# Kernel optimization log

Measured on AMD Instinct MI355X. Metric: run time of the kernel, lower is better.

The kernel has to match this reference:

```python
import jax, jax.numpy as jnp
import numpy as np

TAU = 0.01
RHO = 1.99
SIGMA = 1.0 / TAU / 72.0  # 1/tau/72 as in __init__
N_IT = 10  # n_it_max


def nabla2(x):
    # forward finite differences: channel 0 along W (last axis), channel 1 along H
    u = jnp.zeros(x.shape + (2,), x.dtype)
    u = u.at[..., :, :-1, 0].add(x[..., :, 1:] - x[..., :, :-1])
    u = u.at[..., :-1, :, 1].add(x[..., 1:, :] - x[..., :-1, :])
    return u


def nabla2_adjoint(u):
    x = jnp.zeros(u.shape[:-1], u.dtype)
    x = x.at[..., :, :-1].add(-u[..., :, :-1, 0])
    x = x.at[..., :, 1:].add(u[..., :, :-1, 0])
    x = x.at[..., :-1, :].add(-u[..., :-1, :, 1])
    x = x.at[..., 1:, :].add(u[..., :-1, :, 1])
    return x


def epsilon2(I):
    # Jacobian of the vector field I [..., H, W, 2] -> G [..., H, W, 4]
    I0, I1 = I[..., 0], I[..., 1]
    G = jnp.zeros(I0.shape + (4,), I.dtype)
    G = G.at[..., 0].add(I0)                                  # G0 = I0 - shift_H(I0)
    G = G.at[..., 1:, :, 0].add(-I0[..., :-1, :])
    G = G.at[..., :, 1:, 1].add(I0[..., :, 1:] - I0[..., :, :-1])  # G1: W-diff of I0
    G = G.at[..., 2].add(I1)                                  # G2 = I1 - shift_W(I1)
    G = G.at[..., :, 1:, 2].add(-I1[..., :, :-1])
    G = G.at[..., :-1, :, 3].add(I1[..., 1:, :] - I1[..., :-1, :])  # G3: H-diff of I1
    return G


def epsilon2_adjoint(G):
    I = jnp.zeros(G.shape[:-1] + (2,), G.dtype)
    I = I.at[..., 0].add(G[..., 0])
    I = I.at[..., :-1, :, 0].add(-G[..., 1:, :, 0])
    I = I.at[..., :, :-1, 0].add(-G[..., :, 1:, 1])
    I = I.at[..., :, 1:, 0].add(G[..., :, 1:, 1])
    I = I.at[..., 1].add(G[..., 2])
    I = I.at[..., :, :-1, 1].add(-G[..., :, 1:, 2])
    I = I.at[..., :-1, :, 1].add(-G[..., :-1, :, 3])
    I = I.at[..., 1:, :, 1].add(G[..., :-1, :, 3])
    return I


def setup_inputs() -> dict:
    key = jax.random.key(0)
    y = jax.random.normal(key, (4, 512, 512), dtype=jnp.float32)
    return {"y": y, "ths": 1}


def reference(y, ths):
    lam1 = ths * 0.1
    lam2 = ths * 0.15

    def prox_tau_fr(r):
        left = jnp.sqrt(jnp.sum(r * r, axis=-1)) / (TAU * lam1)
        return r - r / jnp.maximum(left, 1.0)[..., None]

    def prox_sigma_g_conj(u):
        return u / jnp.maximum(jnp.sqrt(jnp.sum(u * u, axis=-1)) / lam2, 1.0)[..., None]

    x2 = y
    r2 = jnp.zeros(y.shape + (2,), y.dtype)
    u2 = jnp.zeros(y.shape + (4,), y.dtype)

    def step(carry, _):
        x2, r2, u2 = carry
        tmp = TAU * epsilon2_adjoint(u2)
        x = (x2 - nabla2_adjoint(tmp) + TAU * y) / (1.0 + TAU)  # prox_tau_fx
        r = prox_tau_fr(r2 + tmp)
        u = prox_sigma_g_conj(
            u2 + SIGMA * epsilon2(nabla2(2.0 * x - x2) - (2.0 * r - r2))
        )
        x2 = x2 + RHO * (x - x2)
        r2 = r2 + RHO * (r - r2)
        u2 = u2 + RHO * (u - u2)
        return (x2, r2, u2), None

    (x2, r2, u2), _ = jax.lax.scan(step, (x2, r2, u2), None, length=N_IT)
    return x2
```

## Files before the change

### kernel.cpp

```cpp
#include <hip/hip_runtime.h>
#include <hip/hip_fp16.h>
#include <math.h>

#define HH 512
#define WW 512
#define BB 4
#define NPIX (BB * HH * WW)

#define HS 4
#define NSX 9
#define NBAND (HH / HS)
#define NWAVES (NSX * NBAND * BB)
#define NBLK (NWAVES / 4)
#define BPR (NBLK / 8)

constexpr float TAUf   = 0.01f;
constexpr float RHOf   = 1.99f;
constexpr float SIGMAf = (float)(1.0 / 0.01 / 72.0);
constexpr float INV1PT = (float)(1.0 / 1.01);

__device__ __forceinline__ float SD(float v) { return __shfl_down(v, 1, 64); }
__device__ __forceinline__ unsigned SDu(unsigned v) { return __shfl_down(v, 1, 64); }
__device__ __forceinline__ float SUp(float v) { return __shfl_up(v, 1, 64); }

__device__ __forceinline__ int swiz_wid(int bid, int tid) {
    return (((bid & 7) * BPR) + (bid >> 3)) * 4 + (tid >> 6);
}


template <int MODE>
__global__ __launch_bounds__(256) void sweep(
    const float* __restrict__ y, const int* __restrict__ ths_p,
    const uint2* __restrict__ f_in, const uint2* __restrict__ u_in,
    uint2* __restrict__ f_out, uint2* __restrict__ u_out,
    float* __restrict__ xout)
{
    const int tid  = threadIdx.x;
    const int lane = tid & 63;
    const int wid  = swiz_wid(blockIdx.x, tid);
    const int sx   = wid % NSX;
    const int t2   = wid / NSX;
    const int band = t2 & (NBAND - 1);
    const int b    = t2 / NBAND;
    const int R0   = band * HS;
    const int w    = sx * 60 - 2 + lane;
    const int boff = b * (HH * WW);
    const bool wok = ((unsigned)w) < (unsigned)WW;
    const float mA = (w >= 1 && w < WW) ? 1.f : 0.f;
    const float mB = (w >= 0 && w < WW - 1) ? 1.f : 0.f;
    const bool cok = (lane >= 2) && (lane < 62) && (w < WW);

    const float ths  = (float)ths_p[0];
    const float tl1_ = TAUf * (ths * 0.1f);
    const float l2_  = ths * 0.15f;

    float uf0[4], uf1[4], uf2[4], uf3[4];
    unsigned u12r[4];
    float i0r[2], i1r[2];
    float sr[2], t1r[2];
    float v0r[4], v1r[2];
    #pragma unroll
    for (int q = 0; q < 4; ++q) { uf0[q]=uf1[q]=uf2[q]=uf3[q]=0.f; v0r[q]=0.f; u12r[q]=0u; }
    i0r[0]=i0r[1]=i1r[0]=i1r[1]=0.f;
    sr[0]=sr[1]=0.f; t1r[0]=t1r[1]=0.f; v1r[0]=v1r[1]=0.f;

    auto uload = [&](int row) -> uint2 {
        uint2 z; z.x = 0u; z.y = 0u;
        if (((unsigned)row) < (unsigned)HH && wok)
            z = u_in[(size_t)(boff + row * WW + w)];
        return z;
    };
    auto fload = [&](int row) -> uint2 {
        uint2 z; z.x = 0u; z.y = 0u;
        if (((unsigned)row) < (unsigned)HH && wok)
            z = f_in[(size_t)(boff + row * WW + w)];
        return z;
    };
    auto unpk = [&](int slot, uint2 raw) {
        __half2 lo = *(reinterpret_cast<__half2*>(&raw.x));
        __half2 hi = *(reinterpret_cast<__half2*>(&raw.y));
        uf0[slot] = __low2float(lo); uf1[slot] = __high2float(lo);
        uf2[slot] = __low2float(hi); uf3[slot] = __high2float(hi);
        u12r[slot] = (raw.x >> 16) | (raw.y << 16);
    };
    auto compI = [&](int rr, int islot, int c, int d, int uu_) {
        if (((unsigned)rr) < (unsigned)HH) {
            float hD  = (rr < HH - 1) ? 1.f : 0.f;
            unsigned pp = SDu(u12r[c]);
            __half2 ph = *(reinterpret_cast<__half2*>(&pp));
            float u1n = __low2float(ph);
            float u2n = __high2float(ph);
            i0r[islot] = uf0[c] - uf0[d] - u1n + mA * uf1[c];
            i1r[islot] = uf2[c] - u2n - hD * uf3[c] + uf3[uu_];
        } else { i0r[islot] = 0.f; i1r[islot] = 0.f; }
    };

    if (MODE == 2) {
        unpk(2, uload(R0 - 2));
        unpk(3, uload(R0 - 1));
        unpk(0, uload(R0));
        compI(R0 - 1, 1, 3, 0, 2);
        uint2 puA = uload(R0 + 1);
        uint2 puB = uload(R0 + 2);
        uint2 pfA = fload(R0);
        uint2 pfB = fload(R0 + 1);
        #pragma unroll
        for (int k = 0; k < HS; ++k) {
            const int rr = R0 + k;
            unpk((k + 1) & 3, puA);
            puA = puB;
            if (k < HS - 2) puB = uload(R0 + k + 3);
            __half2 lo = *(reinterpret_cast<__half2*>(&pfA.x));
            __half2 hi = *(reinterpret_cast<__half2*>(&pfA.y));
            float x2v = __low2float(lo);
            float yv  = __high2float(hi);
            pfA = pfB;
            if (k < HS - 2) pfB = fload(R0 + k + 2);
            compI(rr, k & 1, k & 3, (k + 1) & 3, (k + 3) & 3);
            float hD = (rr < HH - 1) ? 1.f : 0.f;
            float i0c = i0r[k & 1], i1c = i1r[k & 1], i1u = i1r[(k + 1) & 1];
            float i0l = SUp(i0c);
            float na = TAUf * (mA * i0l - mB * i0c + i1u - hD * i1c);
            float x = (x2v - na + TAUf * yv) * INV1PT;
            if (cok) xout[boff + rr * WW + w] = x2v + RHOf * (x - x2v);
        }
        return;
    }

    auto compS = [&](int rr, int isc, int isp,
                     float yv, float x2v, float r20v, float r21v, unsigned yraw,
                     bool coreRow, float &sOut, float &t0Out, float &t1Out) {
        if (((unsigned)rr) < (unsigned)HH) {
            float hD = (rr < HH - 1) ? 1.f : 0.f;
            float i0c = i0r[isc], i1c = i1r[isc], i1u = i1r[isp];
            float i0l = SUp(i0c);
            float na = TAUf * (mA * i0l - mB * i0c + i1u - hD * i1c);
            float x = (x2v - na + TAUf * yv) * INV1PT;
            float rr0 = r20v + TAUf * i0c;
            float rr1 = r21v + TAUf * i1c;
            float d = rr0 * rr0 + rr1 * rr1;
            float rinv = fminf(tl1_ * __builtin_amdgcn_rsqf(d), 1.0f);
            float r0 = rr0 - rr0 * rinv;
            float r1 = rr1 - rr1 * rinv;
            sOut  = 2.f * x  - x2v;
            t0Out = 2.f * r0 - r20v;
            t1Out = 2.f * r1 - r21v;
            if (coreRow && cok) {
                int idx = boff + rr * WW + w;
                __half2 lo2 = __floats2half2_rn(x2v + RHOf * (x - x2v),
                                                r20v + RHOf * (r0 - r20v));
                unsigned r1b = (unsigned)__half_as_ushort(
                    __float2half(r21v + RHOf * (r1 - r21v)));
                uint2 st; st.x = *(unsigned*)&lo2; st.y = r1b | (yraw << 16);
                f_out[(size_t)idx] = st;
            }
        } else { sOut = 0.f; t0Out = 0.f; t1Out = 0.f; }
    };

    auto compU = [&](int ro, int v0c_s, int v0u_s, int v1c_s, int v1d_s, int uslot) {
        float hD  = (ro < HH - 1) ? 1.f : 0.f;
        float v0c = v0r[v0c_s], v0u = v0r[v0u_s];
        float v1c = v1r[v1c_s], v1d = v1r[v1d_s];
        float v0l = SUp(v0c);
        float v1l = SUp(v1c);
        float G0 = v0c - v0u;
        float G1 = mA * (v0c - v0l);
        float G2 = v1c - mA * v1l;
        float G3 = hD * (v1d - v1c);
        float u0v = uf0[uslot], u1v = uf1[uslot], u2v = uf2[uslot], u3v = uf3[uslot];
        float uu0 = u0v + SIGMAf * G0;
        float uu1 = u1v + SIGMAf * G1;
        float uu2 = u2v + SIGMAf * G2;
        float uu3 = u3v + SIGMAf * G3;
        float d = uu0 * uu0 + uu1 * uu1 + uu2 * uu2 + uu3 * uu3;
        float ui = fminf(l2_ * __builtin_amdgcn_rsqf(d), 1.0f);
        if (cok) {
            int idx = boff + ro * WW + w;
            __half2 lo = __floats2half2_rn(u0v + RHOf * (uu0 * ui - u0v),
                                           u1v + RHOf * (uu1 * ui - u1v));
            __half2 hi = __floats2half2_rn(u2v + RHOf * (uu2 * ui - u2v),
                                           u3v + RHOf * (uu3 * ui - u3v));
            uint2 st; st.x = *(unsigned*)&lo; st.y = *(unsigned*)&hi;
            u_out[(size_t)idx] = st;
        }
    };

    uint2 puA, puB, pfA, pfB;
    puA.x = puA.y = puB.x = puB.y = 0u;
    pfA.x = pfA.y = pfB.x = pfB.y = 0u;
    unpk(1, uload(R0 - 3));
    unpk(2, uload(R0 - 2));
    unpk(3, uload(R0 - 1));
    compI(R0 - 2, 0, 2, 3, 1);
    puA = uload(R0);
    puB = uload(R0 + 1);
    pfA = fload(R0 - 1);
    pfB = fload(R0);

    #pragma unroll
    for (int k = 0; k < HS + 3; ++k) {
        const int rr = R0 - 1 + k;
        unpk(k & 3, puA);
        puA = puB;
        if (k <= HS) puB = uload(R0 + k + 2);
        __half2 lo = *(reinterpret_cast<__half2*>(&pfA.x));
        __half2 hi = *(reinterpret_cast<__half2*>(&pfA.y));
        float x2v  = __low2float(lo);
        float r20v = __high2float(lo);
        float r21v = __low2float(hi);
        float yv   = __high2float(hi);
        unsigned yraw = pfA.y >> 16;
        pfA = pfB;
        if (k <= HS) pfB = fload(R0 + k + 1);

        compI(rr, (k + 1) & 1, (k + 3) & 3, k & 3, (k + 2) & 3);

        float sN, t0N, t1N;
        compS(rr, (k + 1) & 1, k & 1, yv, x2v, r20v, r21v, yraw,
              (k >= 1 && k <= HS), sN, t0N, t1N);

        {
            float sPrev  = sr[k & 1];
            float t1Prev = t1r[k & 1];
            float hDm1   = (rr < HH) ? 1.f : 0.f;
            v0r[(k + 3) & 3] = mB * (SD(sN) - sN) - t0N;
            v1r[k & 1]       = hDm1 * (sN - sPrev) - t1Prev;
            sr[(k + 1) & 1]  = sN;
            t1r[(k + 1) & 1] = t1N;
        }

        if (k >= 3) compU(R0 - 3 + k, (k + 1) & 3, k & 3, (k + 1) & 1, k & 1,
                          (k + 1) & 3);
    }
}

__global__ __launch_bounds__(256) void fused01(
    const float* __restrict__ y, const int* __restrict__ ths_p,
    uint2* __restrict__ f_out, uint2* __restrict__ u_out)
{
    const int tid  = threadIdx.x;
    const int lane = tid & 63;
    const int wid  = swiz_wid(blockIdx.x, tid);
    const int sx   = wid % NSX;
    const int t2   = wid / NSX;
    const int band = t2 & (NBAND - 1);
    const int b    = t2 / NBAND;
    const int R0   = band * HS;
    const int w    = sx * 58 - 3 + lane;
    const int boff = b * (HH * WW);
    const bool wok = ((unsigned)w) < (unsigned)WW;
    const float mA = (w >= 1 && w < WW) ? 1.f : 0.f;
    const float mB = (w >= 0 && w < WW - 1) ? 1.f : 0.f;
    const bool cok = (lane >= 3) && (lane <= 60) && (w < WW);

    const float ths  = (float)ths_p[0];
    const float tl1_ = TAUf * (ths * 0.1f);
    const float l2_  = ths * 0.15f;

    float p0r[4];
    float p1r[2];
    float yD1 = 0.f, yD2 = 0.f, yD3 = 0.f;

    float uf0[4], uf1[4], uf2[4], uf3[4];
    unsigned u12r[4];
    float i0r[2], i1r[2];
    float sr[2], t1r[2];
    float v0r[4], v1r[2];
    #pragma unroll
    for (int q = 0; q < 4; ++q) {
        uf0[q]=uf1[q]=uf2[q]=uf3[q]=0.f; v0r[q]=0.f; u12r[q]=0u; p0r[q]=0.f;
    }
    i0r[0]=i0r[1]=i1r[0]=i1r[1]=0.f;
    sr[0]=sr[1]=0.f; t1r[0]=t1r[1]=0.f; v1r[0]=v1r[1]=0.f; p1r[0]=p1r[1]=0.f;

    auto yload = [&](int row) -> float {
        return (((unsigned)row) < (unsigned)HH && wok)
                   ? y[boff + row * WW + w] : 0.f;
    };
    auto unpk = [&](int slot, uint2 raw) {
        __half2 lo = *(reinterpret_cast<__half2*>(&raw.x));
        __half2 hi = *(reinterpret_cast<__half2*>(&raw.y));
        uf0[slot] = __low2float(lo); uf1[slot] = __high2float(lo);
        uf2[slot] = __low2float(hi); uf3[slot] = __high2float(hi);
        u12r[slot] = (raw.x >> 16) | (raw.y << 16);
    };
    auto compI = [&](int rr, int islot, int c, int d, int uu_) {
        if (((unsigned)rr) < (unsigned)HH) {
            float hD  = (rr < HH - 1) ? 1.f : 0.f;
            unsigned pp = SDu(u12r[c]);
            __half2 ph = *(reinterpret_cast<__half2*>(&pp));
            float u1n = __low2float(ph);
            float u2n = __high2float(ph);
            i0r[islot] = uf0[c] - uf0[d] - u1n + mA * uf1[c];
            i1r[islot] = uf2[c] - u2n - hD * uf3[c] + uf3[uu_];
        } else { i0r[islot] = 0.f; i1r[islot] = 0.f; }
    };

    float pyA = yload(R0 - 4);
    float pyB = yload(R0 - 3);

    #pragma unroll
    for (int j = 0; j < HS + 9; ++j) {
        const int p = R0 - 4 + j;
        float yp = pyA; pyA = pyB;
        if (j <= HS + 6) pyB = yload(R0 - 2 + j);

        p0r[j & 3]       = mB * (SD(yp) - yp);
        p1r[(j + 1) & 1] = ((p < HH) ? 1.f : 0.f) * (yp - yD1);

        if (j >= 3) {
            const int ro = R0 - 6 + j;
            float hD  = (ro < HH - 1) ? 1.f : 0.f;
            float v0c = p0r[(j + 2) & 3], v0u = p0r[(j + 1) & 3];
            float v1c = p1r[j & 1],       v1d = p1r[(j + 1) & 1];
            float G0 = v0c - v0u;
            float G1 = mA * (v0c - SUp(v0c));
            float G2 = v1c - mA * SUp(v1c);
            float G3 = hD * (v1d - v1c);
            float uu0 = SIGMAf * G0, uu1 = SIGMAf * G1;
            float uu2 = SIGMAf * G2, uu3 = SIGMAf * G3;
            float d = uu0*uu0 + uu1*uu1 + uu2*uu2 + uu3*uu3;
            float ui = fminf(l2_ * __builtin_amdgcn_rsqf(d), 1.0f);
            __half2 lo = __floats2half2_rn(RHOf * (uu0 * ui), RHOf * (uu1 * ui));
            __half2 hi = __floats2half2_rn(RHOf * (uu2 * ui), RHOf * (uu3 * ui));
            uint2 st; st.x = *(unsigned*)&lo; st.y = *(unsigned*)&hi;
            unpk((j + 2) & 3, st);
        }

        if (j == 5) compI(R0 - 2, 0, 2, 3, 1);

        if (j >= 6) {
            const int k  = j - 6;
            const int rr = R0 - 1 + k;
            __half yh = __float2half(yD3);
            float yv  = __half2float(yh);
            unsigned yraw = (unsigned)__half_as_ushort(yh);

            compI(rr, (k + 1) & 1, (k + 3) & 3, k & 3, (k + 2) & 3);

            float sN, t0N, t1N;
            {
                const bool coreRow = (k >= 1 && k <= HS);
                if (((unsigned)rr) < (unsigned)HH) {
                    float hD = (rr < HH - 1) ? 1.f : 0.f;
                    float i0c = i0r[(k + 1) & 1], i1c = i1r[(k + 1) & 1];
                    float i1u = i1r[k & 1];
                    float i0l = SUp(i0c);
                    float na = TAUf * (mA * i0l - mB * i0c + i1u - hD * i1c);
                    float x = (yv - na + TAUf * yv) * INV1PT;
                    float rr0 = TAUf * i0c;
                    float rr1 = TAUf * i1c;
                    float d2 = rr0*rr0 + rr1*rr1;
                    float rinv = fminf(tl1_ * __builtin_amdgcn_rsqf(d2), 1.0f);
                    float r0 = rr0 - rr0 * rinv;
                    float r1 = rr1 - rr1 * rinv;
                    sN  = 2.f * x - yv;
                    t0N = 2.f * r0;
                    t1N = 2.f * r1;
                    if (coreRow && cok) {
                        int idx = boff + rr * WW + w;
                        __half2 lo2 = __floats2half2_rn(yv + RHOf * (x - yv),
                                                        RHOf * r0);
                        unsigned r1b = (unsigned)__half_as_ushort(
                            __float2half(RHOf * r1));
                        uint2 st2; st2.x = *(unsigned*)&lo2;
                        st2.y = r1b | (yraw << 16);
                        f_out[(size_t)idx] = st2;
                    }
                } else { sN = 0.f; t0N = 0.f; t1N = 0.f; }
            }

            {
                float sPrev  = sr[k & 1];
                float t1Prev = t1r[k & 1];
                float hDm1   = (rr < HH) ? 1.f : 0.f;
                v0r[(k + 3) & 3] = mB * (SD(sN) - sN) - t0N;
                v1r[k & 1]       = hDm1 * (sN - sPrev) - t1Prev;
                sr[(k + 1) & 1]  = sN;
                t1r[(k + 1) & 1] = t1N;
            }

            if (k >= 3) {
                const int ro = R0 - 3 + k;
                float hD  = (ro < HH - 1) ? 1.f : 0.f;
                float v0c = v0r[(k + 1) & 3], v0u = v0r[k & 3];
                float v1c = v1r[(k + 1) & 1], v1d = v1r[k & 1];
                float v0l = SUp(v0c);
                float v1l = SUp(v1c);
                float G0 = v0c - v0u;
                float G1 = mA * (v0c - v0l);
                float G2 = v1c - mA * v1l;
                float G3 = hD * (v1d - v1c);
                const int us = (k + 1) & 3;
                float u0v = uf0[us], u1v = uf1[us], u2v = uf2[us], u3v = uf3[us];
                float uu0 = u0v + SIGMAf * G0;
                float uu1 = u1v + SIGMAf * G1;
                float uu2 = u2v + SIGMAf * G2;
                float uu3 = u3v + SIGMAf * G3;
                float d = uu0*uu0 + uu1*uu1 + uu2*uu2 + uu3*uu3;
                float ui = fminf(l2_ * __builtin_amdgcn_rsqf(d), 1.0f);
                if (cok) {
                    int idx = boff + ro * WW + w;
                    __half2 lo = __floats2half2_rn(u0v + RHOf * (uu0 * ui - u0v),
                                                   u1v + RHOf * (uu1 * ui - u1v));
                    __half2 hi = __floats2half2_rn(u2v + RHOf * (uu2 * ui - u2v),
                                                   u3v + RHOf * (uu3 * ui - u3v));
                    uint2 st; st.x = *(unsigned*)&lo; st.y = *(unsigned*)&hi;
                    u_out[(size_t)idx] = st;
                }
            }
        }

        yD3 = yD2; yD2 = yD1; yD1 = yp;
    }
}

__global__ __launch_bounds__(256) void fused89(
    const int* __restrict__ ths_p,
    const uint2* __restrict__ f_in, const uint2* __restrict__ u_in,
    float* __restrict__ xout)
{
    const int tid  = threadIdx.x;
    const int lane = tid & 63;
    const int wid  = swiz_wid(blockIdx.x, tid);
    const int sx   = wid % NSX;
    const int t2   = wid / NSX;
    const int band = t2 & (NBAND - 1);
    const int b    = t2 / NBAND;
    const int R0   = band * HS;
    const int R0p  = R0 - 2;
    const int w    = sx * 58 - 3 + lane;
    const int boff = b * (HH * WW);
    const bool wok = ((unsigned)w) < (unsigned)WW;
    const float mA = (w >= 1 && w < WW) ? 1.f : 0.f;
    const float mB = (w >= 0 && w < WW - 1) ? 1.f : 0.f;
    const bool cokC = (lane >= 3) && (lane <= 60) && (w < WW);

    const float ths  = (float)ths_p[0];
    const float tl1_ = TAUf * (ths * 0.1f);
    const float l2_  = ths * 0.15f;

    constexpr int HSp = HS + 3;

    float uf0[4], uf1[4], uf2[4], uf3[4];
    unsigned u12r[4];
    float i0r[2], i1r[2];
    float sr[2], t1r[2];
    float v0r[4], v1r[2];
    float cf0[4], cf1[4], cf2[4], cf3[4];
    unsigned c12[4];
    float ci0[2], ci1[2];
    uint2 fmid[4];
    #pragma unroll
    for (int q = 0; q < 4; ++q) {
        uf0[q]=uf1[q]=uf2[q]=uf3[q]=0.f; v0r[q]=0.f; u12r[q]=0u;
        cf0[q]=cf1[q]=cf2[q]=cf3[q]=0.f; c12[q]=0u;
        fmid[q].x = 0u; fmid[q].y = 0u;
    }
    i0r[0]=i0r[1]=i1r[0]=i1r[1]=0.f;
    ci0[0]=ci0[1]=ci1[0]=ci1[1]=0.f;
    sr[0]=sr[1]=0.f; t1r[0]=t1r[1]=0.f; v1r[0]=v1r[1]=0.f;

    auto uload = [&](int row) -> uint2 {
        uint2 z; z.x = 0u; z.y = 0u;
        if (((unsigned)row) < (unsigned)HH && wok)
            z = u_in[(size_t)(boff + row * WW + w)];
        return z;
    };
    auto fload = [&](int row) -> uint2 {
        uint2 z; z.x = 0u; z.y = 0u;
        if (((unsigned)row) < (unsigned)HH && wok)
            z = f_in[(size_t)(boff + row * WW + w)];
        return z;
    };
    auto unpk = [&](int slot, uint2 raw) {
        __half2 lo = *(reinterpret_cast<__half2*>(&raw.x));
        __half2 hi = *(reinterpret_cast<__half2*>(&raw.y));
        uf0[slot] = __low2float(lo); uf1[slot] = __high2float(lo);
        uf2[slot] = __low2float(hi); uf3[slot] = __high2float(hi);
        u12r[slot] = (raw.x >> 16) | (raw.y << 16);
    };
    auto compI = [&](int rr, int islot, int c, int d, int uu_) {
        if (((unsigned)rr) < (unsigned)HH) {
            float hD  = (rr < HH - 1) ? 1.f : 0.f;
            unsigned pp = SDu(u12r[c]);
            __half2 ph = *(reinterpret_cast<__half2*>(&pp));
            float u1n = __low2float(ph);
            float u2n = __high2float(ph);
            i0r[islot] = uf0[c] - uf0[d] - u1n + mA * uf1[c];
            i1r[islot] = uf2[c] - u2n - hD * uf3[c] + uf3[uu_];
        } else { i0r[islot] = 0.f; i1r[islot] = 0.f; }
    };
    auto cunpk = [&](int slot, uint2 raw) {
        __half2 lo = *(reinterpret_cast<__half2*>(&raw.x));
        __half2 hi = *(reinterpret_cast<__half2*>(&raw.y));
        cf0[slot] = __low2float(lo); cf1[slot] = __high2float(lo);
        cf2[slot] = __low2float(hi); cf3[slot] = __high2float(hi);
        c12[slot] = (raw.x >> 16) | (raw.y << 16);
    };
    auto ccompI = [&](int rr, int islot, int c, int d, int uu_) {
        if (((unsigned)rr) < (unsigned)HH) {
            float hD  = (rr < HH - 1) ? 1.f : 0.f;
            unsigned pp = SDu(c12[c]);
            __half2 ph = *(reinterpret_cast<__half2*>(&pp));
            float u1n = __low2float(ph);
            float u2n = __high2float(ph);
            ci0[islot] = cf0[c] - cf0[d] - u1n + mA * cf1[c];
            ci1[islot] = cf2[c] - u2n - hD * cf3[c] + cf3[uu_];
        } else { ci0[islot] = 0.f; ci1[islot] = 0.f; }
    };

    unpk(1, uload(R0p - 3));
    unpk(2, uload(R0p - 2));
    unpk(3, uload(R0p - 1));
    compI(R0p - 2, 0, 2, 3, 1);
    uint2 puA = uload(R0p);
    uint2 puB = uload(R0p + 1);
    uint2 pfA = fload(R0p - 1);
    uint2 pfB = fload(R0p);

    #pragma unroll
    for (int J = 0; J < HSp + 3; ++J) {
        const int rp = R0p - 1 + J;

        unpk(J & 3, puA);
        puA = puB;
        if (J <= HSp) puB = uload(R0p + J + 2);
        __half2 flo = *(reinterpret_cast<__half2*>(&pfA.x));
        __half2 fhi = *(reinterpret_cast<__half2*>(&pfA.y));
        float x2v  = __low2float(flo);
        float r20v = __high2float(flo);
        float r21v = __low2float(fhi);
        float yv   = __high2float(fhi);
        unsigned yraw = pfA.y >> 16;
        pfA = pfB;
        if (J <= HSp) pfB = fload(R0p + J + 1);

        compI(rp, (J + 1) & 1, (J + 3) & 3, J & 3, (J + 2) & 3);

        float sN, t0N, t1N;
        if (((unsigned)rp) < (unsigned)HH) {
            float hD = (rp < HH - 1) ? 1.f : 0.f;
            float i0c = i0r[(J + 1) & 1], i1c = i1r[(J + 1) & 1];
            float i1u = i1r[J & 1];
            float i0l = SUp(i0c);
            float na = TAUf * (mA * i0l - mB * i0c + i1u - hD * i1c);
            float x = (x2v - na + TAUf * yv) * INV1PT;
            float rr0 = r20v + TAUf * i0c;
            float rr1 = r21v + TAUf * i1c;
            float d = rr0 * rr0 + rr1 * rr1;
            float rinv = fminf(tl1_ * __builtin_amdgcn_rsqf(d), 1.0f);
            float r0 = rr0 - rr0 * rinv;
            float r1 = rr1 - rr1 * rinv;
            sN  = 2.f * x  - x2v;
            t0N = 2.f * r0 - r20v;
            t1N = 2.f * r1 - r21v;
            if (J >= 3 && J <= HS + 2) {
                __half2 lo2 = __floats2half2_rn(x2v + RHOf * (x - x2v),
                                                r20v + RHOf * (r0 - r20v));
                unsigned r1b = (unsigned)__half_as_ushort(
                    __float2half(r21v + RHOf * (r1 - r21v)));
                uint2 st; st.x = *(unsigned*)&lo2; st.y = r1b | (yraw << 16);
                fmid[(J + 1) & 3] = st;
            }
        } else { sN = 0.f; t0N = 0.f; t1N = 0.f; }

        {
            float sPrev  = sr[J & 1];
            float t1Prev = t1r[J & 1];
            float hDm1   = (rp < HH) ? 1.f : 0.f;
            v0r[(J + 3) & 3] = mB * (SD(sN) - sN) - t0N;
            v1r[J & 1]       = hDm1 * (sN - sPrev) - t1Prev;
            sr[(J + 1) & 1]  = sN;
            t1r[(J + 1) & 1] = t1N;
        }

        if (J >= 3) {
            const int ro = R0p - 3 + J;
            float hD  = (ro < HH - 1) ? 1.f : 0.f;
            float v0c = v0r[(J + 1) & 3], v0u = v0r[J & 3];
            float v1c = v1r[(J + 1) & 1], v1d = v1r[J & 1];
            float v0l = SUp(v0c);
            float v1l = SUp(v1c);
            float G0 = v0c - v0u;
            float G1 = mA * (v0c - v0l);
            float G2 = v1c - mA * v1l;
            float G3 = hD * (v1d - v1c);
            const int us = (J + 1) & 3;
            float u0v = uf0[us], u1v = uf1[us], u2v = uf2[us], u3v = uf3[us];
            float uu0 = u0v + SIGMAf * G0;
            float uu1 = u1v + SIGMAf * G1;
            float uu2 = u2v + SIGMAf * G2;
            float uu3 = u3v + SIGMAf * G3;
            float d = uu0*uu0 + uu1*uu1 + uu2*uu2 + uu3*uu3;
            float ui = fminf(l2_ * __builtin_amdgcn_rsqf(d), 1.0f);
            uint2 st; st.x = 0u; st.y = 0u;
            if (((unsigned)ro) < (unsigned)HH) {
                __half2 lo = __floats2half2_rn(u0v + RHOf * (uu0 * ui - u0v),
                                               u1v + RHOf * (uu1 * ui - u1v));
                __half2 hi = __floats2half2_rn(u2v + RHOf * (uu2 * ui - u2v),
                                               u3v + RHOf * (uu3 * ui - u3v));
                st.x = *(unsigned*)&lo; st.y = *(unsigned*)&hi;
            }
            cunpk((J + 3) & 3, st);
        }

        if (J == 5) ccompI(R0 - 1, 1, 3, 0, 2);
        if (J >= 6) {
            const int kc = J - 6;
            const int rc = R0 + kc;
            ccompI(rc, kc & 1, kc & 3, (kc + 1) & 3, (kc + 3) & 3);
            uint2 fm = fmid[(J + 2) & 3];
            __half2 mlo = *(reinterpret_cast<__half2*>(&fm.x));
            __half2 mhi = *(reinterpret_cast<__half2*>(&fm.y));
            float cx2 = __low2float(mlo);
            float cyv = __high2float(mhi);
            float hD = (rc < HH - 1) ? 1.f : 0.f;
            float i0c = ci0[kc & 1], i1c = ci1[kc & 1], i1u = ci1[(kc + 1) & 1];
            float i0l = SUp(i0c);
            float na = TAUf * (mA * i0l - mB * i0c + i1u - hD * i1c);
            float x = (cx2 - na + TAUf * cyv) * INV1PT;
            if (cokC) xout[boff + rc * WW + w] = cx2 + RHOf * (x - cx2);
        }
    }
}

extern "C" void kernel_launch(void* const* d_in, const int* in_sizes, int n_in,
                              void* d_out, int out_size, void* d_ws, size_t ws_size,
                              hipStream_t stream)
{
    const float* y   = (const float*)d_in[0];
    const int*   ths = (const int*)d_in[1];
    uint2* ws2 = (uint2*)d_ws;

    uint2* FA = ws2;
    uint2* UA = ws2 + (size_t)NPIX;
    uint2* FB = ws2 + 2 * (size_t)NPIX;
    uint2* UB = ws2 + 3 * (size_t)NPIX;
    float* xout = (float*)d_out;

    dim3 block(256);
    dim3 grid(NBLK);

    fused01<<<grid, block, 0, stream>>>(y, ths, FA, UA);
    uint2 *fi = FA, *ui = UA, *fo = FB, *uo = UB;
    for (int it = 2; it <= 7; ++it) {
        sweep<1><<<grid, block, 0, stream>>>(y, ths, fi, ui, fo, uo, nullptr);
        uint2* t;
        t = fi; fi = fo; fo = t;
        t = ui; ui = uo; uo = t;
    }
    fused89<<<grid, block, 0, stream>>>(ths, fi, ui, xout);
}
```

Measured before the change: 137.3 us.

## Fuse pairs of middle iterations into one temporally-blocked sweep kernel

Replaces the six single-iteration sweep launches with three fusedMM launches, each computing two PDHG iterations per pass. The intermediate f and u state is kept in registers across the two iterations, and tiles widen their halo (56-column core, 10 tiles per row, taller row window) to cover the second iteration's dependencies. This halves global-memory round trips and launch count for iterations 2-7. The cost is redundant halo recomputation, more blocks, and much higher register pressure, which may lower occupancy.

```diff
diff --git a/kernel.cpp b/kernel.cpp
--- a/kernel.cpp
+++ b/kernel.cpp
@@ -14,6 +14,11 @@
 #define NBLK (NWAVES / 4)
 #define BPR (NBLK / 8)
 
+#define NSXP 10
+#define NWAVESP (NSXP * NBAND * BB)
+#define NBLKP (NWAVESP / 4)
+#define BPRP (NBLKP / 8)
+
 constexpr float TAUf   = 0.01f;
 constexpr float RHOf   = 1.99f;
 constexpr float SIGMAf = (float)(1.0 / 0.01 / 72.0);
@@ -23,216 +28,6 @@
 __device__ __forceinline__ unsigned SDu(unsigned v) { return __shfl_down(v, 1, 64); }
 __device__ __forceinline__ float SUp(float v) { return __shfl_up(v, 1, 64); }
 
-__device__ __forceinline__ int swiz_wid(int bid, int tid) {
-    return (((bid & 7) * BPR) + (bid >> 3)) * 4 + (tid >> 6);
-}
-
-
-template <int MODE>
-__global__ __launch_bounds__(256) void sweep(
-    const float* __restrict__ y, const int* __restrict__ ths_p,
-    const uint2* __restrict__ f_in, const uint2* __restrict__ u_in,
-    uint2* __restrict__ f_out, uint2* __restrict__ u_out,
-    float* __restrict__ xout)
-{
-    const int tid  = threadIdx.x;
-    const int lane = tid & 63;
-    const int wid  = swiz_wid(blockIdx.x, tid);
-    const int sx   = wid % NSX;
-    const int t2   = wid / NSX;
-    const int band = t2 & (NBAND - 1);
-    const int b    = t2 / NBAND;
-    const int R0   = band * HS;
-    const int w    = sx * 60 - 2 + lane;
-    const int boff = b * (HH * WW);
-    const bool wok = ((unsigned)w) < (unsigned)WW;
-    const float mA = (w >= 1 && w < WW) ? 1.f : 0.f;
-    const float mB = (w >= 0 && w < WW - 1) ? 1.f : 0.f;
-    const bool cok = (lane >= 2) && (lane < 62) && (w < WW);
-
-    const float ths  = (float)ths_p[0];
-    const float tl1_ = TAUf * (ths * 0.1f);
-    const float l2_  = ths * 0.15f;
-
-    float uf0[4], uf1[4], uf2[4], uf3[4];
-    unsigned u12r[4];
-    float i0r[2], i1r[2];
-    float sr[2], t1r[2];
-    float v0r[4], v1r[2];
-    #pragma unroll
-    for (int q = 0; q < 4; ++q) { uf0[q]=uf1[q]=uf2[q]=uf3[q]=0.f; v0r[q]=0.f; u12r[q]=0u; }
-    i0r[0]=i0r[1]=i1r[0]=i1r[1]=0.f;
-    sr[0]=sr[1]=0.f; t1r[0]=t1r[1]=0.f; v1r[0]=v1r[1]=0.f;
-
-    auto uload = [&](int row) -> uint2 {
-        uint2 z; z.x = 0u; z.y = 0u;
-        if (((unsigned)row) < (unsigned)HH && wok)
-            z = u_in[(size_t)(boff + row * WW + w)];
-        return z;
-    };
-    auto fload = [&](int row) -> uint2 {
-        uint2 z; z.x = 0u; z.y = 0u;
-        if (((unsigned)row) < (unsigned)HH && wok)
-            z = f_in[(size_t)(boff + row * WW + w)];
-        return z;
-    };
-    auto unpk = [&](int slot, uint2 raw) {
-        __half2 lo = *(reinterpret_cast<__half2*>(&raw.x));
-        __half2 hi = *(reinterpret_cast<__half2*>(&raw.y));
-        uf0[slot] = __low2float(lo); uf1[slot] = __high2float(lo);
-        uf2[slot] = __low2float(hi); uf3[slot] = __high2float(hi);
-        u12r[slot] = (raw.x >> 16) | (raw.y << 16);
-    };
-    auto compI = [&](int rr, int islot, int c, int d, int uu_) {
-        if (((unsigned)rr) < (unsigned)HH) {
-            float hD  = (rr < HH - 1) ? 1.f : 0.f;
-            unsigned pp = SDu(u12r[c]);
-            __half2 ph = *(reinterpret_cast<__half2*>(&pp));
-            float u1n = __low2float(ph);
-            float u2n = __high2float(ph);
-            i0r[islot] = uf0[c] - uf0[d] - u1n + mA * uf1[c];
-            i1r[islot] = uf2[c] - u2n - hD * uf3[c] + uf3[uu_];
-        } else { i0r[islot] = 0.f; i1r[islot] = 0.f; }
-    };
-
-    if (MODE == 2) {
-        unpk(2, uload(R0 - 2));
-        unpk(3, uload(R0 - 1));
-        unpk(0, uload(R0));
-        compI(R0 - 1, 1, 3, 0, 2);
-        uint2 puA = uload(R0 + 1);
-        uint2 puB = uload(R0 + 2);
-        uint2 pfA = fload(R0);
-        uint2 pfB = fload(R0 + 1);
-        #pragma unroll
-        for (int k = 0; k < HS; ++k) {
-            const int rr = R0 + k;
-            unpk((k + 1) & 3, puA);
-            puA = puB;
-            if (k < HS - 2) puB = uload(R0 + k + 3);
-            __half2 lo = *(reinterpret_cast<__half2*>(&pfA.x));
-            __half2 hi = *(reinterpret_cast<__half2*>(&pfA.y));
-            float x2v = __low2float(lo);
-            float yv  = __high2float(hi);
-            pfA = pfB;
-            if (k < HS - 2) pfB = fload(R0 + k + 2);
-            compI(rr, k & 1, k & 3, (k + 1) & 3, (k + 3) & 3);
-            float hD = (rr < HH - 1) ? 1.f : 0.f;
-            float i0c = i0r[k & 1], i1c = i1r[k & 1], i1u = i1r[(k + 1) & 1];
-            float i0l = SUp(i0c);
-            float na = TAUf * (mA * i0l - mB * i0c + i1u - hD * i1c);
-            float x = (x2v - na + TAUf * yv) * INV1PT;
-            if (cok) xout[boff + rr * WW + w] = x2v + RHOf * (x - x2v);
-        }
-        return;
-    }
-
-    auto compS = [&](int rr, int isc, int isp,
-                     float yv, float x2v, float r20v, float r21v, unsigned yraw,
-                     bool coreRow, float &sOut, float &t0Out, float &t1Out) {
-        if (((unsigned)rr) < (unsigned)HH) {
-            float hD = (rr < HH - 1) ? 1.f : 0.f;
-            float i0c = i0r[isc], i1c = i1r[isc], i1u = i1r[isp];
-            float i0l = SUp(i0c);
-            float na = TAUf * (mA * i0l - mB * i0c + i1u - hD * i1c);
-            float x = (x2v - na + TAUf * yv) * INV1PT;
-            float rr0 = r20v + TAUf * i0c;
-            float rr1 = r21v + TAUf * i1c;
-            float d = rr0 * rr0 + rr1 * rr1;
-            float rinv = fminf(tl1_ * __builtin_amdgcn_rsqf(d), 1.0f);
-            float r0 = rr0 - rr0 * rinv;
-            float r1 = rr1 - rr1 * rinv;
-            sOut  = 2.f * x  - x2v;
-            t0Out = 2.f * r0 - r20v;
-            t1Out = 2.f * r1 - r21v;
-            if (coreRow && cok) {
-                int idx = boff + rr * WW + w;
-                __half2 lo2 = __floats2half2_rn(x2v + RHOf * (x - x2v),
-                                                r20v + RHOf * (r0 - r20v));
-                unsigned r1b = (unsigned)__half_as_ushort(
-                    __float2half(r21v + RHOf * (r1 - r21v)));
-                uint2 st; st.x = *(unsigned*)&lo2; st.y = r1b | (yraw << 16);
-                f_out[(size_t)idx] = st;
-            }
-        } else { sOut = 0.f; t0Out = 0.f; t1Out = 0.f; }
-    };
-
-    auto compU = [&](int ro, int v0c_s, int v0u_s, int v1c_s, int v1d_s, int uslot) {
-        float hD  = (ro < HH - 1) ? 1.f : 0.f;
-        float v0c = v0r[v0c_s], v0u = v0r[v0u_s];
-        float v1c = v1r[v1c_s], v1d = v1r[v1d_s];
-        float v0l = SUp(v0c);
-        float v1l = SUp(v1c);
-        float G0 = v0c - v0u;
-        float G1 = mA * (v0c - v0l);
-        float G2 = v1c - mA * v1l;
-        float G3 = hD * (v1d - v1c);
-        float u0v = uf0[uslot], u1v = uf1[uslot], u2v = uf2[uslot], u3v = uf3[uslot];
-        float uu0 = u0v + SIGMAf * G0;
-        float uu1 = u1v + SIGMAf * G1;
-        float uu2 = u2v + SIGMAf * G2;
-        float uu3 = u3v + SIGMAf * G3;
-        float d = uu0 * uu0 + uu1 * uu1 + uu2 * uu2 + uu3 * uu3;
-        float ui = fminf(l2_ * __builtin_amdgcn_rsqf(d), 1.0f);
-        if (cok) {
-            int idx = boff + ro * WW + w;
-            __half2 lo = __floats2half2_rn(u0v + RHOf * (uu0 * ui - u0v),
-                                           u1v + RHOf * (uu1 * ui - u1v));
-            __half2 hi = __floats2half2_rn(u2v + RHOf * (uu2 * ui - u2v),
-                                           u3v + RHOf * (uu3 * ui - u3v));
-            uint2 st; st.x = *(unsigned*)&lo; st.y = *(unsigned*)&hi;
-            u_out[(size_t)idx] = st;
-        }
-    };
-
-    uint2 puA, puB, pfA, pfB;
-    puA.x = puA.y = puB.x = puB.y = 0u;
-    pfA.x = pfA.y = pfB.x = pfB.y = 0u;
-    unpk(1, uload(R0 - 3));
-    unpk(2, uload(R0 - 2));
-    unpk(3, uload(R0 - 1));
-    compI(R0 - 2, 0, 2, 3, 1);
-    puA = uload(R0);
-    puB = uload(R0 + 1);
-    pfA = fload(R0 - 1);
-    pfB = fload(R0);
-
-    #pragma unroll
-    for (int k = 0; k < HS + 3; ++k) {
-        const int rr = R0 - 1 + k;
-        unpk(k & 3, puA);
-        puA = puB;
-        if (k <= HS) puB = uload(R0 + k + 2);
-        __half2 lo = *(reinterpret_cast<__half2*>(&pfA.x));
-        __half2 hi = *(reinterpret_cast<__half2*>(&pfA.y));
-        float x2v  = __low2float(lo);
-        float r20v = __high2float(lo);
-        float r21v = __low2float(hi);
-        float yv   = __high2float(hi);
-        unsigned yraw = pfA.y >> 16;
-        pfA = pfB;
-        if (k <= HS) pfB = fload(R0 + k + 1);
-
-        compI(rr, (k + 1) & 1, (k + 3) & 3, k & 3, (k + 2) & 3);
-
-        float sN, t0N, t1N;
-        compS(rr, (k + 1) & 1, k & 1, yv, x2v, r20v, r21v, yraw,
-              (k >= 1 && k <= HS), sN, t0N, t1N);
-
-        {
-            float sPrev  = sr[k & 1];
-            float t1Prev = t1r[k & 1];
-            float hDm1   = (rr < HH) ? 1.f : 0.f;
-            v0r[(k + 3) & 3] = mB * (SD(sN) - sN) - t0N;
-            v1r[k & 1]       = hDm1 * (sN - sPrev) - t1Prev;
-            sr[(k + 1) & 1]  = sN;
-            t1r[(k + 1) & 1] = t1N;
-        }
-
-        if (k >= 3) compU(R0 - 3 + k, (k + 1) & 3, k & 3, (k + 1) & 1, k & 1,
-                          (k + 1) & 3);
-    }
-}
 
 __global__ __launch_bounds__(256) void fused01(
     const float* __restrict__ y, const int* __restrict__ ths_p,
@@ -240,7 +35,8 @@
 {
     const int tid  = threadIdx.x;
     const int lane = tid & 63;
-    const int wid  = swiz_wid(blockIdx.x, tid);
+    const int bid  = blockIdx.x;
+    const int wid  = (((bid & 7) * BPR) + (bid >> 3)) * 4 + (tid >> 6);
     const int sx   = wid % NSX;
     const int t2   = wid / NSX;
     const int band = t2 & (NBAND - 1);
@@ -415,6 +211,285 @@
     }
 }
 
+__global__ __launch_bounds__(256) void fusedMM(
+    const int* __restrict__ ths_p,
+    const uint2* __restrict__ f_in, const uint2* __restrict__ u_in,
+    uint2* __restrict__ f_out, uint2* __restrict__ u_out)
+{
+    const int tid  = threadIdx.x;
+    const int lane = tid & 63;
+    const int bid  = blockIdx.x;
+    const int wid  = (((bid & 7) * BPRP) + (bid >> 3)) * 4 + (tid >> 6);
+    const int sx   = wid % NSXP;
+    const int t2   = wid / NSXP;
+    const int band = t2 & (NBAND - 1);
+    const int b    = t2 / NBAND;
+    const int R0   = band * HS;
+    const int w    = sx * 56 - 4 + lane;
+    const int boff = b * (HH * WW);
+    const bool wok = ((unsigned)w) < (unsigned)WW;
+    const float mA = (w >= 1 && w < WW) ? 1.f : 0.f;
+    const float mB = (w >= 0 && w < WW - 1) ? 1.f : 0.f;
+    const bool cokC = (lane >= 4) && (lane <= 59) && (w < WW);
+
+    const float ths  = (float)ths_p[0];
+    const float tl1_ = TAUf * (ths * 0.1f);
+    const float l2_  = ths * 0.15f;
+
+    constexpr int HSP = 10;
+
+    float uf0[4], uf1[4], uf2[4], uf3[4];
+    unsigned u12r[4];
+    float i0r[2], i1r[2];
+    float sr[2], t1r[2];
+    float v0r[4], v1r[2];
+    float cf0[4], cf1[4], cf2[4], cf3[4];
+    unsigned c12[4];
+    float ci0[2], ci1[2];
+    float csr[2], ct1r[2];
+    float cv0[4], cv1[2];
+    uint2 fmid[4];
+    #pragma unroll
+    for (int q = 0; q < 4; ++q) {
+        uf0[q]=uf1[q]=uf2[q]=uf3[q]=0.f; v0r[q]=0.f; u12r[q]=0u;
+        cf0[q]=cf1[q]=cf2[q]=cf3[q]=0.f; c12[q]=0u; cv0[q]=0.f;
+        fmid[q].x = 0u; fmid[q].y = 0u;
+    }
+    i0r[0]=i0r[1]=i1r[0]=i1r[1]=0.f;
+    ci0[0]=ci0[1]=ci1[0]=ci1[1]=0.f;
+    sr[0]=sr[1]=0.f; t1r[0]=t1r[1]=0.f; v1r[0]=v1r[1]=0.f;
+    csr[0]=csr[1]=0.f; ct1r[0]=ct1r[1]=0.f; cv1[0]=cv1[1]=0.f;
+
+    auto uload = [&](int row) -> uint2 {
+        uint2 z; z.x = 0u; z.y = 0u;
+        if (((unsigned)row) < (unsigned)HH && wok)
+            z = u_in[(size_t)(boff + row * WW + w)];
+        return z;
+    };
+    auto fload = [&](int row) -> uint2 {
+        uint2 z; z.x = 0u; z.y = 0u;
+        if (((unsigned)row) < (unsigned)HH && wok)
+            z = f_in[(size_t)(boff + row * WW + w)];
+        return z;
+    };
+    auto unpk = [&](int slot, uint2 raw) {
+        __half2 lo = *(reinterpret_cast<__half2*>(&raw.x));
+        __half2 hi = *(reinterpret_cast<__half2*>(&raw.y));
+        uf0[slot] = __low2float(lo); uf1[slot] = __high2float(lo);
+        uf2[slot] = __low2float(hi); uf3[slot] = __high2float(hi);
+        u12r[slot] = (raw.x >> 16) | (raw.y << 16);
+    };
+    auto compI = [&](int rr, int islot, int c, int d, int uu_) {
+        if (((unsigned)rr) < (unsigned)HH) {
+            float hD  = (rr < HH - 1) ? 1.f : 0.f;
+            unsigned pp = SDu(u12r[c]);
+            __half2 ph = *(reinterpret_cast<__half2*>(&pp));
+            float u1n = __low2float(ph);
+            float u2n = __high2float(ph);
+            i0r[islot] = uf0[c] - uf0[d] - u1n + mA * uf1[c];
+            i1r[islot] = uf2[c] - u2n - hD * uf3[c] + uf3[uu_];
+        } else { i0r[islot] = 0.f; i1r[islot] = 0.f; }
+    };
+    auto cunpk = [&](int slot, uint2 raw) {
+        __half2 lo = *(reinterpret_cast<__half2*>(&raw.x));
+        __half2 hi = *(reinterpret_cast<__half2*>(&raw.y));
+        cf0[slot] = __low2float(lo); cf1[slot] = __high2float(lo);
+        cf2[slot] = __low2float(hi); cf3[slot] = __high2float(hi);
+        c12[slot] = (raw.x >> 16) | (raw.y << 16);
+    };
+    auto ccompI = [&](int rr, int islot, int c, int d, int uu_) {
+        if (((unsigned)rr) < (unsigned)HH) {
+            float hD  = (rr < HH - 1) ? 1.f : 0.f;
+            unsigned pp = SDu(c12[c]);
+            __half2 ph = *(reinterpret_cast<__half2*>(&pp));
+            float u1n = __low2float(ph);
+            float u2n = __high2float(ph);
+            ci0[islot] = cf0[c] - cf0[d] - u1n + mA * cf1[c];
+            ci1[islot] = cf2[c] - u2n - hD * cf3[c] + cf3[uu_];
+        } else { ci0[islot] = 0.f; ci1[islot] = 0.f; }
+    };
+
+    unpk(2, uload(R0 - 6));
+    unpk(3, uload(R0 - 5));
+    unpk(0, uload(R0 - 4));
+    compI(R0 - 5, 1, 3, 0, 2);
+    uint2 puA = uload(R0 - 3);
+    uint2 puB = uload(R0 - 2);
+    uint2 pfA = fload(R0 - 4);
+    uint2 pfB = fload(R0 - 3);
+
+    #pragma unroll
+    for (int J = 0; J < HSP + 3; ++J) {
+        const int rp = R0 - 4 + J;
+
+        unpk((J + 1) & 3, puA);
+        puA = puB;
+        if (J <= HSP) puB = uload(R0 - 1 + J);
+        __half2 flo = *(reinterpret_cast<__half2*>(&pfA.x));
+        __half2 fhi = *(reinterpret_cast<__half2*>(&pfA.y));
+        float x2v  = __low2float(flo);
+        float r20v = __high2float(flo);
+        float r21v = __low2float(fhi);
+        float yv   = __high2float(fhi);
+        unsigned yraw = pfA.y >> 16;
+        pfA = pfB;
+        if (J <= HSP) pfB = fload(R0 - 2 + J);
+
+        compI(rp, J & 1, J & 3, (J + 1) & 3, (J + 3) & 3);
+
+        float sN, t0N, t1N;
+        if (((unsigned)rp) < (unsigned)HH) {
+            float hD = (rp < HH - 1) ? 1.f : 0.f;
+            float i0c = i0r[J & 1], i1c = i1r[J & 1];
+            float i1u = i1r[(J + 1) & 1];
+            float i0l = SUp(i0c);
+            float na = TAUf * (mA * i0l - mB * i0c + i1u - hD * i1c);
+            float x = (x2v - na + TAUf * yv) * INV1PT;
+            float rr0 = r20v + TAUf * i0c;
+            float rr1 = r21v + TAUf * i1c;
+            float d = rr0 * rr0 + rr1 * rr1;
+            float rinv = fminf(tl1_ * __builtin_amdgcn_rsqf(d), 1.0f);
+            float r0 = rr0 - rr0 * rinv;
+            float r1 = rr1 - rr1 * rinv;
+            sN  = 2.f * x  - x2v;
+            t0N = 2.f * r0 - r20v;
+            t1N = 2.f * r1 - r21v;
+            if (J >= 3 && J <= 9) {
+                __half2 lo2 = __floats2half2_rn(x2v + RHOf * (x - x2v),
+                                                r20v + RHOf * (r0 - r20v));
+                unsigned r1b = (unsigned)__half_as_ushort(
+                    __float2half(r21v + RHOf * (r1 - r21v)));
+                uint2 st; st.x = *(unsigned*)&lo2; st.y = r1b | (yraw << 16);
+                fmid[J & 3] = st;
+            }
+        } else { sN = 0.f; t0N = 0.f; t1N = 0.f; }
+
+        {
+            float sPrev  = sr[(J + 1) & 1];
+            float t1Prev = t1r[(J + 1) & 1];
+            float hDm1   = (rp < HH) ? 1.f : 0.f;
+            v0r[J & 3]       = mB * (SD(sN) - sN) - t0N;
+            v1r[(J + 1) & 1] = hDm1 * (sN - sPrev) - t1Prev;
+            sr[J & 1]        = sN;
+            t1r[J & 1]       = t1N;
+        }
+
+        if (J >= 3) {
+            const int ro = R0 - 6 + J;
+            float hD  = (ro < HH - 1) ? 1.f : 0.f;
+            float v0c = v0r[(J + 2) & 3], v0u = v0r[(J + 1) & 3];
+            float v1c = v1r[J & 1],       v1d = v1r[(J + 1) & 1];
+            float v0l = SUp(v0c);
+            float v1l = SUp(v1c);
+            float G0 = v0c - v0u;
+            float G1 = mA * (v0c - v0l);
+            float G2 = v1c - mA * v1l;
+            float G3 = hD * (v1d - v1c);
+            const int us = (J + 2) & 3;
+            float u0v = uf0[us], u1v = uf1[us], u2v = uf2[us], u3v = uf3[us];
+            float uu0 = u0v + SIGMAf * G0;
+            float uu1 = u1v + SIGMAf * G1;
+            float uu2 = u2v + SIGMAf * G2;
+            float uu3 = u3v + SIGMAf * G3;
+            float d = uu0*uu0 + uu1*uu1 + uu2*uu2 + uu3*uu3;
+            float ui = fminf(l2_ * __builtin_amdgcn_rsqf(d), 1.0f);
+            uint2 st; st.x = 0u; st.y = 0u;
+            if (((unsigned)ro) < (unsigned)HH) {
+                __half2 lo = __floats2half2_rn(u0v + RHOf * (uu0 * ui - u0v),
+                                               u1v + RHOf * (uu1 * ui - u1v));
+                __half2 hi = __floats2half2_rn(u2v + RHOf * (uu2 * ui - u2v),
+                                               u3v + RHOf * (uu3 * ui - u3v));
+                st.x = *(unsigned*)&lo; st.y = *(unsigned*)&hi;
+            }
+            cunpk((J + 2) & 3, st);
+        }
+
+        if (J == 5) ccompI(R0 - 2, 0, 2, 3, 1);
+        if (J >= 6) {
+            const int kc = J - 6;
+            const int rc = R0 - 1 + kc;
+            ccompI(rc, (kc + 1) & 1, (kc + 3) & 3, kc & 3, (kc + 2) & 3);
+
+            uint2 fm = fmid[(kc + 3) & 3];
+            __half2 mlo = *(reinterpret_cast<__half2*>(&fm.x));
+            __half2 mhi = *(reinterpret_cast<__half2*>(&fm.y));
+            float cx2  = __low2float(mlo);
+            float cr0  = __high2float(mlo);
+            float cr1  = __low2float(mhi);
+            float cyv  = __high2float(mhi);
+            unsigned cyraw = fm.y >> 16;
+
+            float csN, ct0N, ct1N;
+            if (((unsigned)rc) < (unsigned)HH) {
+                float hD = (rc < HH - 1) ? 1.f : 0.f;
+                float i0c = ci0[(kc + 1) & 1], i1c = ci1[(kc + 1) & 1];
+                float i1u = ci1[kc & 1];
+                float i0l = SUp(i0c);
+                float na = TAUf * (mA * i0l - mB * i0c + i1u - hD * i1c);
+                float x = (cx2 - na + TAUf * cyv) * INV1PT;
+                float rr0 = cr0 + TAUf * i0c;
+                float rr1 = cr1 + TAUf * i1c;
+                float d = rr0 * rr0 + rr1 * rr1;
+                float rinv = fminf(tl1_ * __builtin_amdgcn_rsqf(d), 1.0f);
+                float r0 = rr0 - rr0 * rinv;
+                float r1 = rr1 - rr1 * rinv;
+                csN  = 2.f * x  - cx2;
+                ct0N = 2.f * r0 - cr0;
+                ct1N = 2.f * r1 - cr1;
+                if (kc >= 1 && kc <= HS && cokC) {
+                    int idx = boff + rc * WW + w;
+                    __half2 lo2 = __floats2half2_rn(cx2 + RHOf * (x - cx2),
+                                                    cr0 + RHOf * (r0 - cr0));
+                    unsigned r1b = (unsigned)__half_as_ushort(
+                        __float2half(cr1 + RHOf * (r1 - cr1)));
+                    uint2 st; st.x = *(unsigned*)&lo2; st.y = r1b | (cyraw << 16);
+                    f_out[(size_t)idx] = st;
+                }
+            } else { csN = 0.f; ct0N = 0.f; ct1N = 0.f; }
+
+            {
+                float sPrev  = csr[kc & 1];
+                float t1Prev = ct1r[kc & 1];
+                float hDm1   = (rc < HH) ? 1.f : 0.f;
+                cv0[(kc + 3) & 3] = mB * (SD(csN) - csN) - ct0N;
+                cv1[kc & 1]       = hDm1 * (csN - sPrev) - t1Prev;
+                csr[(kc + 1) & 1] = csN;
+                ct1r[(kc + 1) & 1]= ct1N;
+            }
+
+            if (kc >= 3) {
+                const int ro = R0 - 3 + kc;
+                float hD  = (ro < HH - 1) ? 1.f : 0.f;
+                float v0c = cv0[(kc + 1) & 3], v0u = cv0[kc & 3];
+                float v1c = cv1[(kc + 1) & 1], v1d = cv1[kc & 1];
+                float v0l = SUp(v0c);
+                float v1l = SUp(v1c);
+                float G0 = v0c - v0u;
+                float G1 = mA * (v0c - v0l);
+                float G2 = v1c - mA * v1l;
+                float G3 = hD * (v1d - v1c);
+                const int us = (kc + 1) & 3;
+                float u0v = cf0[us], u1v = cf1[us], u2v = cf2[us], u3v = cf3[us];
+                float uu0 = u0v + SIGMAf * G0;
+                float uu1 = u1v + SIGMAf * G1;
+                float uu2 = u2v + SIGMAf * G2;
+                float uu3 = u3v + SIGMAf * G3;
+                float d = uu0*uu0 + uu1*uu1 + uu2*uu2 + uu3*uu3;
+                float ui = fminf(l2_ * __builtin_amdgcn_rsqf(d), 1.0f);
+                if (cokC) {
+                    int idx = boff + ro * WW + w;
+                    __half2 lo = __floats2half2_rn(u0v + RHOf * (uu0 * ui - u0v),
+                                                   u1v + RHOf * (uu1 * ui - u1v));
+                    __half2 hi = __floats2half2_rn(u2v + RHOf * (uu2 * ui - u2v),
+                                                   u3v + RHOf * (uu3 * ui - u3v));
+                    uint2 st; st.x = *(unsigned*)&lo; st.y = *(unsigned*)&hi;
+                    u_out[(size_t)idx] = st;
+                }
+            }
+        }
+    }
+}
+
 __global__ __launch_bounds__(256) void fused89(
     const int* __restrict__ ths_p,
     const uint2* __restrict__ f_in, const uint2* __restrict__ u_in,
@@ -422,7 +497,8 @@
 {
     const int tid  = threadIdx.x;
     const int lane = tid & 63;
-    const int wid  = swiz_wid(blockIdx.x, tid);
+    const int bid  = blockIdx.x;
+    const int wid  = (((bid & 7) * BPR) + (bid >> 3)) * 4 + (tid >> 6);
     const int sx   = wid % NSX;
     const int t2   = wid / NSX;
     const int band = t2 & (NBAND - 1);
@@ -640,15 +716,10 @@
     float* xout = (float*)d_out;
 
     dim3 block(256);
-    dim3 grid(NBLK);
-
-    fused01<<<grid, block, 0, stream>>>(y, ths, FA, UA);
-    uint2 *fi = FA, *ui = UA, *fo = FB, *uo = UB;
-    for (int it = 2; it <= 7; ++it) {
-        sweep<1><<<grid, block, 0, stream>>>(y, ths, fi, ui, fo, uo, nullptr);
-        uint2* t;
-        t = fi; fi = fo; fo = t;
-        t = ui; ui = uo; uo = t;
-    }
-    fused89<<<grid, block, 0, stream>>>(ths, fi, ui, xout);
+
+    fused01<<<dim3(NBLK), block, 0, stream>>>(y, ths, FA, UA);
+    fusedMM<<<dim3(NBLKP), block, 0, stream>>>(ths, FA, UA, FB, UB);
+    fusedMM<<<dim3(NBLKP), block, 0, stream>>>(ths, FB, UB, FA, UA);
+    fusedMM<<<dim3(NBLKP), block, 0, stream>>>(ths, FA, UA, FB, UB);
+    fused89<<<dim3(NBLK), block, 0, stream>>>(ths, FB, UB, xout);
 }
```

After: 137.0 us. Within noise of the previous version (-0.2%).
